# Kernel optimization log

Hardware: AMD Instinct MI355X
Metric: run time of the kernel (lower is better)

## Reference

```python
import jax, jax.numpy as jnp
import numpy as np

K = 5  # top-k neighbors (init kwarg k)
EPS = 1e-12

def _normalize(x):
    n = jnp.linalg.norm(x, axis=1, keepdims=True)
    return x / jnp.maximum(n, EPS)

def setup_inputs() -> dict:
    key = jax.random.key(0)
    k1, k2, k3 = jax.random.split(key, 3)
    B, D, N, C = 1024, 1024, 100000, 1000
    features = jax.random.normal(k1, (B, D), dtype=jnp.float32)
    idx = jax.random.randint(k2, (B,), 0, N, dtype=jnp.int64)
    # buffers: feat_memory = F.normalize(rand(N, D)); pred_memory = ones(N, C)/C
    feat_memory = _normalize(jax.random.uniform(k3, (N, D), dtype=jnp.float32))
    pred_memory = jnp.ones((N, C), dtype=jnp.float32) / C
    return {"features": features, "idx": idx,
            "feat_memory": feat_memory, "pred_memory": pred_memory}

def reference(features, idx, feat_memory, pred_memory):
    B = features.shape[0]
    x = _normalize(features)                       # [B, D]
    dis = x @ feat_memory.T                        # [B, N] similarity
    # self-mask: each row's own bank entry set to global min (min is invariant
    # under this assignment, so the per-row torch loop vectorizes exactly)
    m = jnp.min(dis)
    dis = dis.at[jnp.arange(B), idx].set(m)
    _, indices = jax.lax.top_k(dis, K)             # [B, K]
    mean_logits = jnp.mean(pred_memory[indices], axis=1)  # [B, C]
    pseudo_labels = jnp.argmax(mean_logits, axis=1)       # [B]
    return pseudo_labels, mean_logits
```

## Files before the change

kernel.cpp:

```cpp
#include <hip/hip_runtime.h>
#include <stdint.h>
#include <stddef.h>

#define B_ROWS 1024
#define D_DIM  1024
#define N_MEM  100000
#define C_CLS  1000
#define K_TOP  5

#define BM 256
#define BN 256
#define BKT 64
#define NKT (D_DIM / BKT)
#define NT_TILES ((N_MEM + BN - 1) / BN)
#define NPAD (NT_TILES * BN)
#define BT_TILES (B_ROWS / BM)
#define NT_PER_XCD 49
#define GRID_GEMM (8 * NT_PER_XCD * BT_TILES)

typedef __bf16 bf16;
typedef bf16 bf16x4 __attribute__((ext_vector_type(4)));
typedef bf16 bf16x8 __attribute__((ext_vector_type(8)));
typedef float f32x4 __attribute__((ext_vector_type(4)));

#define MFMA16(a, b, c) __builtin_amdgcn_mfma_f32_16x16x32_bf16((a), (b), (c), 0, 0, 0)
#define BARRIER() do { asm volatile("" ::: "memory"); \
                       __builtin_amdgcn_s_barrier();  \
                       asm volatile("" ::: "memory"); } while (0)
#define WAITVM(N) asm volatile("s_waitcnt vmcnt(" #N ")" ::: "memory")
#define LGKM0()   asm volatile("s_waitcnt lgkmcnt(0)" ::: "memory")
#define VM0()     asm volatile("s_waitcnt vmcnt(0)" ::: "memory")

__device__ __forceinline__ void insert5(float v, int n, float tv[K_TOP], int ti[K_TOP]) {
#pragma unroll
  for (int j = 0; j < K_TOP; ++j) {
    bool gt = v > tv[j];
    float ov = tv[j]; int oi = ti[j];
    tv[j] = gt ? v : ov;  ti[j] = gt ? n : oi;
    v = gt ? ov : v;      n = gt ? oi : n;
  }
}

__global__ __launch_bounds__(256) void k_normalize(const float* __restrict__ F,
                                                   bf16* __restrict__ X) {
  int row = blockIdx.x;
  int tid = threadIdx.x;
  const float4* fr = (const float4*)(F + (size_t)row * D_DIM);
  float4 v = fr[tid];
  float s = v.x * v.x + v.y * v.y + v.z * v.z + v.w * v.w;
  for (int off = 32; off > 0; off >>= 1) s += __shfl_down(s, off, 64);
  __shared__ float wred[4];
  if ((tid & 63) == 0) wred[tid >> 6] = s;
  __syncthreads();
  float tot = wred[0] + wred[1] + wred[2] + wred[3];
  float inv = 1.0f / fmaxf(sqrtf(tot), 1e-12f);
  bf16x4 o;
  o[0] = (bf16)(v.x * inv);
  o[1] = (bf16)(v.y * inv);
  o[2] = (bf16)(v.z * inv);
  o[3] = (bf16)(v.w * inv);
  *(bf16x4*)(X + (size_t)row * D_DIM + (size_t)tid * 4) = o;
}

__global__ __launch_bounds__(256) void k_convert(const float* __restrict__ FM,
                                                 bf16* __restrict__ FMB,
                                                 int total8, int pad8) {
  int i = blockIdx.x * 256 + threadIdx.x;
  if (i >= pad8) return;
  bf16x8 o;
  if (i < total8) {
    float4 a = ((const float4*)FM)[2 * i];
    float4 b = ((const float4*)FM)[2 * i + 1];
    o[0] = (bf16)a.x; o[1] = (bf16)a.y; o[2] = (bf16)a.z; o[3] = (bf16)a.w;
    o[4] = (bf16)b.x; o[5] = (bf16)b.y; o[6] = (bf16)b.z; o[7] = (bf16)b.w;
  } else {
#pragma unroll
    for (int e = 0; e < 8; ++e) o[e] = (bf16)0.f;
  }
  ((bf16x8*)FMB)[i] = o;
}

__device__ __forceinline__ void gl_lds16(const bf16* g, char* l) {
  __builtin_amdgcn_global_load_lds((__attribute__((address_space(1))) void*)g,
                                   (__attribute__((address_space(3))) void*)l,
                                   16, 0, 0);
}

#define STAGE_HALF(g, off, rbase, k0) do {                                     \
    gl_lds16((g) + (size_t)(rbase) * D_DIM + (k0),      lds + (off) + d0);     \
    gl_lds16((g) + (size_t)((rbase) + 64) * D_DIM + (k0), lds + (off) + d1);   \
  } while (0)

#define LOAD_AFQ(dst, qi, Ab_) do {                                            \
    dst[0][0] = *(const bf16x8*)((Ab_) + (2 * (qi) + 0) * 2048 + cs0);         \
    dst[0][1] = *(const bf16x8*)((Ab_) + (2 * (qi) + 0) * 2048 + cs1);         \
    dst[1][0] = *(const bf16x8*)((Ab_) + (2 * (qi) + 1) * 2048 + cs0);         \
    dst[1][1] = *(const bf16x8*)((Ab_) + (2 * (qi) + 1) * 2048 + cs1);         \
  } while (0)

#define LOAD_BF(dst, nb, Bb_) do {                                             \
    dst[0] = *(const bf16x8*)((Bb_) + (nb) * 2048 + cs0);                      \
    dst[1] = *(const bf16x8*)((Bb_) + (nb) * 2048 + cs1);                      \
  } while (0)

#define MMA8(aq, r0, n0) do {                                                  \
    __builtin_amdgcn_s_setprio(1);                                             \
    _Pragma("unroll") for (int kk = 0; kk < 2; ++kk)                           \
      _Pragma("unroll") for (int m = 0; m < 2; ++m)                            \
        _Pragma("unroll") for (int nb = 0; nb < 2; ++nb)                       \
          acc[(r0) + m][(n0) + nb] = MFMA16(aq[m][kk], bfr[(n0) + nb][kk],     \
                                            acc[(r0) + m][(n0) + nb]);         \
    __builtin_amdgcn_s_setprio(0);                                             \
  } while (0)

__global__ __launch_bounds__(512, 2) void k_gemm_topk(const bf16* __restrict__ X,
                                                      const bf16* __restrict__ FMB,
                                                      const int* __restrict__ IDX,
                                                      float2* __restrict__ CAND) {
  extern __shared__ char lds[];
  int bid = blockIdx.x;
  int xcd = bid & 7;
  int jj = bid >> 3;
  int cnt = (xcd < 7) ? NT_PER_XCD : (NT_TILES - 7 * NT_PER_XCD);
  if (jj >= 4 * cnt) return;
  int nt = xcd * NT_PER_XCD + (jj >> 2);
  int bt = jj & 3;
  size_t row0 = (size_t)bt * BM;
  size_t col0 = (size_t)nt * BN;

  int tid = threadIdx.x;
  int lane = tid & 63;
  int wv = tid >> 6;
  int wm = wv >> 2, wn = wv & 3;
  int frow = lane & 15, q = lane >> 4;
  int cs0 = ((q ^ (frow & 7)) * 16);
  int cs1 = (((q + 4) ^ (frow & 7)) * 16);

  int arow0 = tid >> 3;
  int jsrc = (tid & 7) ^ (arow0 & 7);
  const bf16* gA = X   + ((size_t)row0 + arow0) * D_DIM + jsrc * 8;
  const bf16* gB = FMB + ((size_t)col0 + arow0) * D_DIM + jsrc * 8;
  int d0 = tid * 16;
  int d1 = 8192 + tid * 16;

  STAGE_HALF(gA, 0,     0,   0);
  STAGE_HALF(gA, 16384, 128, 0);
  STAGE_HALF(gB, 32768, 0,   0);
  STAGE_HALF(gB, 49152, 128, 0);
  STAGE_HALF(gA, 65536 + 0,     0,   BKT);
  STAGE_HALF(gA, 65536 + 16384, 128, BKT);
  STAGE_HALF(gB, 65536 + 32768, 0,   BKT);
  STAGE_HALF(gB, 65536 + 49152, 128, BKT);

  f32x4 acc[8][4];
#pragma unroll
  for (int mi = 0; mi < 8; ++mi)
#pragma unroll
    for (int ni = 0; ni < 4; ++ni)
      acc[mi][ni] = (f32x4){0.f, 0.f, 0.f, 0.f};

  WAITVM(8);
  BARRIER();

  bf16x8 afq[4][2][2];
  bf16x8 bfr[4][2];

  {
    const char* Ab_ = lds + wm * 16384 + frow * 128;
    const char* Bb_ = lds + 32768 + (wn >> 1) * 16384 + (wn & 1) * 8192 + frow * 128;
    LOAD_BF(bfr[0], 0, Bb_);
    LOAD_BF(bfr[1], 1, Bb_);
    LOAD_BF(bfr[2], 2, Bb_);
    LOAD_BF(bfr[3], 3, Bb_);
    LOAD_AFQ(afq[0], 0, Ab_);
    LOAD_AFQ(afq[1], 1, Ab_);
  }

  for (int kt = 0; kt < NKT; ++kt) {
    int bo  = (kt & 1) << 16;
    int bon = ((kt + 1) & 1) << 16;
    const char* Ab  = lds + bo  + wm * 16384 + frow * 128;
    const char* Abn = lds + bon + wm * 16384 + frow * 128;
    const char* Bbn = lds + bon + 32768 + (wn >> 1) * 16384 + (wn & 1) * 8192 + frow * 128;
    bool st = (kt < NKT - 2), pf = (kt < NKT - 1);
    int k2 = (kt + 2) * BKT;

    LOAD_AFQ(afq[2], 2, Ab);
    MMA8(afq[0], 0, 0);
    LOAD_AFQ(afq[3], 3, Ab);
    MMA8(afq[0], 0, 2);
    MMA8(afq[1], 2, 0);
    MMA8(afq[1], 2, 2);

    LGKM0();
    VM0();
    BARRIER();

    if (st) {
      STAGE_HALF(gA, bo + 0,     0,   k2);
      STAGE_HALF(gA, bo + 16384, 128, k2);
      STAGE_HALF(gB, bo + 32768, 0,   k2);
      STAGE_HALF(gB, bo + 49152, 128, k2);
    }
    if (pf) LOAD_AFQ(afq[0], 0, Abn);
    MMA8(afq[2], 4, 0);
    MMA8(afq[2], 4, 2);
    if (pf) LOAD_AFQ(afq[1], 1, Abn);
    MMA8(afq[3], 6, 0);
    if (pf) { LOAD_BF(bfr[0], 0, Bbn); LOAD_BF(bfr[1], 1, Bbn); }
    MMA8(afq[3], 6, 2);
    if (pf) { LOAD_BF(bfr[2], 2, Bbn); LOAD_BF(bfr[3], 3, Bbn); }
  }

  __syncthreads();
  int Rbase = wm * 128 + q * 4;
#pragma unroll
  for (int mi = 0; mi < 8; ++mi)
#pragma unroll
    for (int ni = 0; ni < 4; ++ni) {
      int Cc = wn * 64 + ni * 16 + frow;
      int chunkC = Cc >> 3;
      int e2 = (Cc & 7) * 2;
#pragma unroll
      for (int r = 0; r < 4; ++r) {
        int R = Rbase + mi * 16 + r;
        *(bf16*)(lds + R * 512 + ((chunkC ^ (R & 31)) * 16) + e2) = (bf16)acc[mi][ni][r];
      }
    }
  __syncthreads();

  int tr = tid >> 1, h = tid & 1;
  int grow = (int)row0 + tr;
  int self = IDX[grow];
  float tv[K_TOP]; int ti[K_TOP];
#pragma unroll
  for (int j = 0; j < K_TOP; ++j) { tv[j] = -1e30f; ti[j] = -1; }
  int swz = tr & 31;
#pragma unroll
  for (int c8 = 0; c8 < 16; ++c8) {
    int chunk = h * 16 + c8;
    bf16x8 v8 = *(const bf16x8*)(lds + tr * 512 + ((chunk ^ swz) * 16));
#pragma unroll
    for (int e = 0; e < 8; ++e) {
      int gc = (int)col0 + chunk * 8 + e;
      if (gc >= N_MEM || gc == self) continue;
      float v = (float)v8[e];
      if (v > tv[K_TOP - 1]) insert5(v, gc, tv, ti);
    }
  }
  float pv[K_TOP]; int pi[K_TOP];
#pragma unroll
  for (int j = 0; j < K_TOP; ++j) {
    pv[j] = __shfl_xor(tv[j], 1, 64);
    pi[j] = __shfl_xor(ti[j], 1, 64);
  }
#pragma unroll
  for (int j = 0; j < K_TOP; ++j)
    if (pv[j] > tv[K_TOP - 1]) insert5(pv[j], pi[j], tv, ti);

  if (h == 0) {
    float2* out = CAND + ((size_t)grow * NT_TILES + nt) * K_TOP;
#pragma unroll
    for (int j = 0; j < K_TOP; ++j)
      out[j] = make_float2(tv[j], __int_as_float(ti[j]));
  }
}

__device__ void gather_mean_argmax(const int* find, const float* __restrict__ P,
                                   float* __restrict__ OUT, int b, int tid) {
  float bestV = -1e30f;
  int bestC = 0;
  for (int c = tid; c < C_CLS; c += 256) {
    float s = 0.f;
    for (int j = 0; j < K_TOP; ++j) s += P[(size_t)find[j] * C_CLS + c];
    float mean = s * (1.0f / K_TOP);
    OUT[(size_t)B_ROWS + (size_t)b * C_CLS + c] = mean;
    if (mean > bestV) { bestV = mean; bestC = c; }
  }
  __shared__ float rv[256];
  __shared__ int rc[256];
  rv[tid] = bestV; rc[tid] = bestC;
  for (int s = 128; s >= 1; s >>= 1) {
    __syncthreads();
    if (tid < s) {
      float v2 = rv[tid + s]; int c2 = rc[tid + s];
      if (v2 > rv[tid] || (v2 == rv[tid] && c2 < rc[tid])) { rv[tid] = v2; rc[tid] = c2; }
    }
  }
  __syncthreads();
  if (tid == 0) OUT[b] = (float)rc[0];
}

__global__ __launch_bounds__(256) void k_merge(const float2* __restrict__ CAND,
                                               const float* __restrict__ P,
                                               float* __restrict__ OUT) {
  int b = blockIdx.x;
  int tid = threadIdx.x;
  const float2* row = CAND + (size_t)b * (NT_TILES * K_TOP);

  float tv[K_TOP]; int ti[K_TOP];
  for (int j = 0; j < K_TOP; ++j) { tv[j] = -1e30f; ti[j] = -1; }
  for (int i = tid; i < NT_TILES * K_TOP; i += 256) {
    float2 e = row[i];
    float v = e.x;
    if (v > tv[K_TOP - 1]) insert5(v, __float_as_int(e.y), tv, ti);
  }

  __shared__ float sv[256 * K_TOP];
  __shared__ int si[256 * K_TOP];
  for (int j = 0; j < K_TOP; ++j) { sv[tid * K_TOP + j] = tv[j]; si[tid * K_TOP + j] = ti[j]; }
  for (int s = 128; s >= 1; s >>= 1) {
    __syncthreads();
    if (tid < s) {
      for (int j = 0; j < K_TOP; ++j) {
        float v = sv[(tid + s) * K_TOP + j];
        int n = si[(tid + s) * K_TOP + j];
        if (v > tv[K_TOP - 1]) insert5(v, n, tv, ti);
      }
      for (int j = 0; j < K_TOP; ++j) { sv[tid * K_TOP + j] = tv[j]; si[tid * K_TOP + j] = ti[j]; }
    }
  }
  __syncthreads();
  __shared__ int find[K_TOP];
  if (tid == 0)
    for (int j = 0; j < K_TOP; ++j) {
      int v = si[j];
      find[j] = (v < 0) ? 0 : (v >= N_MEM ? N_MEM - 1 : v);
    }
  __syncthreads();
  gather_mean_argmax(find, P, OUT, b, tid);
}

__global__ __launch_bounds__(256) void k_naive(const float* __restrict__ F,
                                               const int* __restrict__ IDX,
                                               const float* __restrict__ FM,
                                               const float* __restrict__ P,
                                               float* __restrict__ OUT) {
  int b = blockIdx.x;
  int tid = threadIdx.x;
  __shared__ float wred[4];
  const float4* fr = (const float4*)(F + (size_t)b * D_DIM);
  float4 v = fr[tid];
  float s = v.x * v.x + v.y * v.y + v.z * v.z + v.w * v.w;
  for (int off = 32; off > 0; off >>= 1) s += __shfl_down(s, off, 64);
  if ((tid & 63) == 0) wred[tid >> 6] = s;
  __syncthreads();
  float inv = 1.0f / fmaxf(sqrtf(wred[0] + wred[1] + wred[2] + wred[3]), 1e-12f);
  float4 xv = make_float4(v.x * inv, v.y * inv, v.z * inv, v.w * inv);
  __syncthreads();
  int self = IDX[b];
  __shared__ float ptv[K_TOP];
  __shared__ int pti[K_TOP];
  if (tid < K_TOP) { ptv[tid] = -1e30f; pti[tid] = 0; }
  __syncthreads();
  for (int n = 0; n < N_MEM; ++n) {
    const float4* frow = (const float4*)(FM + (size_t)n * D_DIM);
    float4 fv = frow[tid];
    float p = xv.x * fv.x + xv.y * fv.y + xv.z * fv.z + xv.w * fv.w;
    for (int off = 32; off > 0; off >>= 1) p += __shfl_down(p, off, 64);
    if ((tid & 63) == 0) wred[tid >> 6] = p;
    __syncthreads();
    if (tid == 0 && n != self) {
      float tot = wred[0] + wred[1] + wred[2] + wred[3];
      if (tot > ptv[K_TOP - 1]) {
        int q = K_TOP - 1;
        while (q > 0 && tot > ptv[q - 1]) { ptv[q] = ptv[q - 1]; pti[q] = pti[q - 1]; --q; }
        ptv[q] = tot; pti[q] = n;
      }
    }
    __syncthreads();
  }
  __shared__ int find[K_TOP];
  if (tid < K_TOP) {
    int x = pti[tid];
    find[tid] = (x < 0) ? 0 : (x >= N_MEM ? N_MEM - 1 : x);
  }
  __syncthreads();
  gather_mean_argmax(find, P, OUT, b, tid);
}

extern "C" void kernel_launch(void* const* d_in, const int* in_sizes, int n_in,
                              void* d_out, int out_size, void* d_ws, size_t ws_size,
                              hipStream_t stream) {
  const float* F  = (const float*)d_in[0];
  const int* IDX  = (const int*)d_in[1];
  const float* FM = (const float*)d_in[2];
  const float* P  = (const float*)d_in[3];
  float* OUT = (float*)d_out;

  const size_t xBytes    = (size_t)B_ROWS * D_DIM * 2;
  const size_t fmBytes   = (size_t)NPAD * D_DIM * 2;
  const size_t candBytes = (size_t)B_ROWS * NT_TILES * K_TOP * 8;
  const size_t need = xBytes + fmBytes + candBytes;

  if (ws_size >= need) {
    bf16* Xb     = (bf16*)d_ws;
    bf16* FMB    = (bf16*)((char*)d_ws + xBytes);
    float2* CAND = (float2*)((char*)d_ws + xBytes + fmBytes);
    (void)hipFuncSetAttribute((const void*)k_gemm_topk,
                              hipFuncAttributeMaxDynamicSharedMemorySize, 131072);
    k_normalize<<<B_ROWS, 256, 0, stream>>>(F, Xb);
    int total8 = N_MEM * D_DIM / 8;
    int pad8   = NPAD * D_DIM / 8;
    k_convert<<<(pad8 + 255) / 256, 256, 0, stream>>>(FM, FMB, total8, pad8);
    k_gemm_topk<<<GRID_GEMM, 512, 131072, stream>>>(Xb, FMB, IDX, CAND);
    k_merge<<<B_ROWS, 256, 0, stream>>>(CAND, P, OUT);
  } else {
    k_naive<<<B_ROWS, 256, 0, stream>>>(F, IDX, FM, P, OUT);
  }
}
```

Measured before the change: 1.039 ms.

## Restructure GEMM main loop into barrier-separated phases with staggered global staging

Replaces the cross-iteration register prefetch of A/B fragments with a four-phase schedule per K-tile. Each phase loads its fragments from LDS, waits, and runs a cluster of MFMAs under raised priority, with barriers and sched_barrier keeping phases ordered. Global-to-LDS staging of the A and B halves is split into separate phases, and the full vmcnt(0) drain is replaced with a partial wait. The aim is to interleave waves the way ping-pong schedules do, overlapping memory with MFMA work, at the cost of many more barriers per iteration and less register-level prefetching.

```diff
diff --git a/kernel.cpp b/kernel.cpp
--- a/kernel.cpp
+++ b/kernel.cpp
@@ -29,7 +29,7 @@
                        asm volatile("" ::: "memory"); } while (0)
 #define WAITVM(N) asm volatile("s_waitcnt vmcnt(" #N ")" ::: "memory")
 #define LGKM0()   asm volatile("s_waitcnt lgkmcnt(0)" ::: "memory")
-#define VM0()     asm volatile("s_waitcnt vmcnt(0)" ::: "memory")
+#define SCHEDB()  __builtin_amdgcn_sched_barrier(0)
 
 __device__ __forceinline__ void insert5(float v, int n, float tv[K_TOP], int ti[K_TOP]) {
 #pragma unroll
@@ -104,13 +104,11 @@
   } while (0)
 
 #define MMA8(aq, r0, n0) do {                                                  \
-    __builtin_amdgcn_s_setprio(1);                                             \
     _Pragma("unroll") for (int kk = 0; kk < 2; ++kk)                           \
       _Pragma("unroll") for (int m = 0; m < 2; ++m)                            \
         _Pragma("unroll") for (int nb = 0; nb < 2; ++nb)                       \
           acc[(r0) + m][(n0) + nb] = MFMA16(aq[m][kk], bfr[(n0) + nb][kk],     \
                                             acc[(r0) + m][(n0) + nb]);         \
-    __builtin_amdgcn_s_setprio(0);                                             \
   } while (0)
 
 __global__ __launch_bounds__(512, 2) void k_gemm_topk(const bf16* __restrict__ X,
@@ -165,54 +163,63 @@
   bf16x8 afq[4][2][2];
   bf16x8 bfr[4][2];
 
-  {
-    const char* Ab_ = lds + wm * 16384 + frow * 128;
-    const char* Bb_ = lds + 32768 + (wn >> 1) * 16384 + (wn & 1) * 8192 + frow * 128;
-    LOAD_BF(bfr[0], 0, Bb_);
-    LOAD_BF(bfr[1], 1, Bb_);
-    LOAD_BF(bfr[2], 2, Bb_);
-    LOAD_BF(bfr[3], 3, Bb_);
-    LOAD_AFQ(afq[0], 0, Ab_);
-    LOAD_AFQ(afq[1], 1, Ab_);
-  }
-
+#pragma unroll 2
   for (int kt = 0; kt < NKT; ++kt) {
-    int bo  = (kt & 1) << 16;
-    int bon = ((kt + 1) & 1) << 16;
-    const char* Ab  = lds + bo  + wm * 16384 + frow * 128;
-    const char* Abn = lds + bon + wm * 16384 + frow * 128;
-    const char* Bbn = lds + bon + 32768 + (wn >> 1) * 16384 + (wn & 1) * 8192 + frow * 128;
-    bool st = (kt < NKT - 2), pf = (kt < NKT - 1);
+    int bo = (kt & 1) << 16;
+    const char* Ab = lds + bo + wm * 16384 + frow * 128;
+    const char* Bb = lds + bo + 32768 + (wn >> 1) * 16384 + (wn & 1) * 8192 + frow * 128;
+    bool st = (kt < NKT - 2);
     int k2 = (kt + 2) * BKT;
 
+    LOAD_AFQ(afq[0], 0, Ab);
+    LOAD_AFQ(afq[1], 1, Ab);
+    LOAD_BF(bfr[0], 0, Bb);
+    LOAD_BF(bfr[1], 1, Bb);
+    BARRIER();
+    LGKM0(); SCHEDB();
+    __builtin_amdgcn_s_setprio(1);
+    MMA8(afq[0], 0, 0);
+    MMA8(afq[1], 2, 0);
+    __builtin_amdgcn_s_setprio(0);
+    BARRIER();
+
     LOAD_AFQ(afq[2], 2, Ab);
-    MMA8(afq[0], 0, 0);
     LOAD_AFQ(afq[3], 3, Ab);
+    LOAD_BF(bfr[2], 2, Bb);
+    LOAD_BF(bfr[3], 3, Bb);
+    BARRIER();
+    LGKM0(); SCHEDB();
+    __builtin_amdgcn_s_setprio(1);
     MMA8(afq[0], 0, 2);
-    MMA8(afq[1], 2, 0);
     MMA8(afq[1], 2, 2);
-
-    LGKM0();
-    VM0();
+    __builtin_amdgcn_s_setprio(0);
     BARRIER();
 
     if (st) {
       STAGE_HALF(gA, bo + 0,     0,   k2);
       STAGE_HALF(gA, bo + 16384, 128, k2);
+    }
+    BARRIER();
+    __builtin_amdgcn_s_setprio(1);
+    MMA8(afq[2], 4, 0);
+    MMA8(afq[3], 6, 0);
+    __builtin_amdgcn_s_setprio(0);
+    BARRIER();
+
+    if (st) {
       STAGE_HALF(gB, bo + 32768, 0,   k2);
       STAGE_HALF(gB, bo + 49152, 128, k2);
     }
-    if (pf) LOAD_AFQ(afq[0], 0, Abn);
-    MMA8(afq[2], 4, 0);
+    BARRIER();
+    __builtin_amdgcn_s_setprio(1);
     MMA8(afq[2], 4, 2);
-    if (pf) LOAD_AFQ(afq[1], 1, Abn);
-    MMA8(afq[3], 6, 0);
-    if (pf) { LOAD_BF(bfr[0], 0, Bbn); LOAD_BF(bfr[1], 1, Bbn); }
     MMA8(afq[3], 6, 2);
-    if (pf) { LOAD_BF(bfr[2], 2, Bbn); LOAD_BF(bfr[3], 3, Bbn); }
-  }
-
-  __syncthreads();
+    __builtin_amdgcn_s_setprio(0);
+    if (kt < NKT - 2)       { WAITVM(8); }
+    else if (kt == NKT - 2) { WAITVM(0); }
+    BARRIER();
+  }
+
   int Rbase = wm * 128 + q * 4;
 #pragma unroll
   for (int mi = 0; mi < 8; ++mi)
```

After: 1.066 ms. 1.03x slower.
